# Optimization experiments

Hardware: AMD Instinct MI355X
Metric: run time of the kernel (lower is better)

Reference implementation:

```python
import jax, jax.numpy as jnp
import numpy as np

N_NODES = 100000
N_EDGES = 1600000
IN_FEATS = 256
H_FEATS = 128
N_CLASSES = 40


def setup_inputs() -> dict:
    key = jax.random.key(0)
    ks = jax.random.split(key, 6)
    in_feat = jax.random.normal(ks[0], (N_NODES, IN_FEATS), dtype=jnp.float32)
    src = jax.random.randint(ks[1], (N_EDGES,), 0, N_NODES, dtype=jnp.int32)
    dst = jax.random.randint(ks[2], (N_EDGES,), 0, N_NODES, dtype=jnp.int32)
    # Glorot-ish init for the two GraphConv weights
    W1 = jax.random.normal(ks[3], (IN_FEATS, H_FEATS), dtype=jnp.float32) * (1.0 / np.sqrt(IN_FEATS))
    b1 = jnp.zeros((H_FEATS,), dtype=jnp.float32)
    W2 = jax.random.normal(ks[4], (H_FEATS, N_CLASSES), dtype=jnp.float32) * (1.0 / np.sqrt(H_FEATS))
    b2 = jnp.zeros((N_CLASSES,), dtype=jnp.float32)
    return {"in_feat": in_feat, "src": src, "dst": dst,
            "W1": W1, "b1": b1, "W2": W2, "b2": b2}


def _degree_isqrt(idx, n):
    # degree per node, clamped to >=1 (DGL norm='both' behavior), then ^-1/2
    deg = jax.ops.segment_sum(jnp.ones_like(idx, dtype=jnp.float32), idx, num_segments=n)
    return jax.lax.rsqrt(jnp.maximum(deg, 1.0))


def _graph_conv(x, W, b, src, dst, out_isqrt, in_isqrt, n):
    # DGL GraphConv norm='both', weight applied before aggregation
    h = (x @ W) * out_isqrt[:, None]            # [N, F_out]
    m = jax.ops.segment_sum(h[src], dst, num_segments=n)  # gather+scatter over edges
    return m * in_isqrt[:, None] + b


def reference(in_feat, src, dst, W1, b1, W2, b2):
    n = in_feat.shape[0]
    out_isqrt = _degree_isqrt(src, n)  # out-degree norm for source nodes
    in_isqrt = _degree_isqrt(dst, n)   # in-degree norm for destination nodes
    h = _graph_conv(in_feat, W1, b1, src, dst, out_isqrt, in_isqrt, n)
    h = jax.nn.relu(h)
    h = _graph_conv(h, W2, b2, src, dst, out_isqrt, in_isqrt, n)
    return h
```

## Files before the change

### kernel.cpp

```cpp
#include <hip/hip_runtime.h>
#include <hip/hip_bf16.h>
#include <stdint.h>

#define NN 100000
#define NE 1600000
#define INF 256
#define HF 128
#define NC 40
#define NNP 100352
#define NBUK 1568
#define BKSH 6
#define NBLK 256
#define CHUNK 6250
#define SA 1536
#define SB 1536

typedef unsigned short ushort_t;
typedef unsigned int uint_t;
typedef unsigned char uchar_t;
typedef __attribute__((ext_vector_type(8))) short short8;
typedef __attribute__((ext_vector_type(4))) float f32x4;

__device__ __forceinline__ float bflo(uint_t u) {
    union { uint_t i; float f; } v; v.i = u << 16; return v.f;
}
__device__ __forceinline__ float bfhi(uint_t u) {
    union { uint_t i; float f; } v; v.i = u & 0xffff0000u; return v.f;
}
__device__ __forceinline__ uint_t f2bf(float f) {
    __hip_bfloat16 h = __float2bfloat16(f);
    return (uint_t)*reinterpret_cast<ushort_t*>(&h);
}

__global__ void k_binit(uint_t* __restrict__ cursA, uint_t* __restrict__ cursB) {
    int t = blockIdx.x * 256 + threadIdx.x;
    if (t < NBUK) { cursA[t] = (uint_t)t * SA; cursB[t] = (uint_t)t * SB; }
}

__launch_bounds__(1024)
__global__ void k_bfill(const int* __restrict__ src, const int* __restrict__ dst,
                        uint_t* __restrict__ cursA, uint_t* __restrict__ cursB,
                        uint_t* __restrict__ edgesA, uchar_t* __restrict__ bytesB,
                        const float* __restrict__ W1, ushort_t* __restrict__ W1f,
                        const float* __restrict__ W2, ushort_t* __restrict__ W2f) {
    __shared__ uint_t hA[NBUK], hB[NBUK];
    for (int t = threadIdx.x; t < NBUK; t += 1024) { hA[t] = 0; hB[t] = 0; }

    int i = blockIdx.x * 1024 + threadIdx.x;
    if (i < INF * HF) {
        int k = i >> 7, n = i & 127;
        int ks = k >> 5, q = (k >> 3) & 3, j = k & 7;
        int ct = n >> 4, ln = n & 15;
        W1f[(((ks * 8 + ct) * 4 + q) * 16 + ln) * 8 + j] = (ushort_t)f2bf(W1[i]);
    }
    if (i < HF * 48) {
        int k = i / 48, n = i % 48;
        int ks = k >> 5, q = (k >> 3) & 3, j = k & 7;
        int ct = n >> 4, ln = n & 15;
        float v = (n < NC) ? W2[k * NC + n] : 0.0f;
        W2f[(((ks * 3 + ct) * 4 + q) * 16 + ln) * 8 + j] = (ushort_t)f2bf(v);
    }
    __syncthreads();

    const int beg = blockIdx.x * CHUNK, end = beg + CHUNK;
    for (int e = beg + threadIdx.x; e < end; e += 1024) {
        atomicAdd(&hA[(uint_t)dst[e] >> BKSH], 1u);
        atomicAdd(&hB[(uint_t)src[e] >> BKSH], 1u);
    }
    __syncthreads();
    for (int t = threadIdx.x; t < NBUK; t += 1024) {
        uint_t c = hA[t];
        hA[t] = c ? atomicAdd(&cursA[t], c) : 0;
        c = hB[t];
        hB[t] = c ? atomicAdd(&cursB[t], c) : 0;
    }
    __syncthreads();
    for (int e = beg + threadIdx.x; e < end; e += 1024) {
        uint_t d = (uint_t)dst[e], s = (uint_t)src[e];
        uint_t pA = atomicAdd(&hA[d >> BKSH], 1u);
        edgesA[pA] = ((d & 63u) << 17) | s;
        uint_t pB = atomicAdd(&hB[s >> BKSH], 1u);
        bytesB[pB] = (uchar_t)(s & 63u);
    }
}

__launch_bounds__(256)
__global__ void k_bfinish(const uint_t* __restrict__ cursA, const uint_t* __restrict__ cursB,
                          const uint_t* __restrict__ edgesA, const uchar_t* __restrict__ bytesB,
                          int* __restrict__ row_ptr, int* __restrict__ srcs,
                          float* __restrict__ isq_d, float* __restrict__ isq_s) {
    __shared__ uint_t red[256];
    __shared__ uint_t h[64], sc[64], cur[64];
    const int b = blockIdx.x, t = threadIdx.x;

    uint_t acc = 0;
    for (int i = t; i < b; i += 256) acc += cursA[i] - (uint_t)i * SA;
    red[t] = acc;
    __syncthreads();
    for (int off = 128; off > 0; off >>= 1) {
        if (t < off) red[t] += red[t + off];
        __syncthreads();
    }
    const uint_t obase = red[0];

    if (t < 64) h[t] = 0;
    __syncthreads();
    const uint_t begI = (uint_t)b * SA;
    const uint_t endI = cursA[b];
    for (uint_t e = begI + t; e < endI; e += 256)
        atomicAdd(&h[(edgesA[e] >> 17) & 63u], 1u);
    __syncthreads();
    uint_t v = (t < 64) ? h[t] : 0;
    if (t < 64) sc[t] = v;
    __syncthreads();
    for (int off = 1; off < 64; off <<= 1) {
        uint_t tv = (t >= off && t < 64) ? sc[t - off] : 0;
        __syncthreads();
        if (t < 64) sc[t] += tv;
        __syncthreads();
    }
    if (t < 64) {
        uint_t excl = sc[t] - v;
        row_ptr[b * 64 + t] = (int)(obase + excl);
        isq_d[b * 64 + t] = rsqrtf(fmaxf((float)v, 1.0f));
        cur[t] = excl;
    }
    __syncthreads();
    for (uint_t e = begI + t; e < endI; e += 256) {
        uint_t u = edgesA[e];
        uint_t p = atomicAdd(&cur[(u >> 17) & 63u], 1u);
        srcs[obase + p] = (int)(u & 0x1FFFFu);
    }
    __syncthreads();
    if (t < 64) h[t] = 0;
    __syncthreads();
    const uint_t begB = (uint_t)b * SB;
    const uint_t endB = cursB[b];
    for (uint_t e = begB + t; e < endB; e += 256)
        atomicAdd(&h[bytesB[e]], 1u);
    __syncthreads();
    if (t < 64) isq_s[b * 64 + t] = rsqrtf(fmaxf((float)h[t], 1.0f));
}

__launch_bounds__(256, 4)
__global__ void k_gemm1(const float* __restrict__ X, const ushort_t* __restrict__ W1f,
                        const float* __restrict__ isq_s, ushort_t* __restrict__ H) {
    const int wv = threadIdx.x >> 6;
    const int lane = threadIdx.x & 63;
    const int ln = lane & 15;
    const int q  = lane >> 4;
    const int r0 = blockIdx.x * 64 + wv * 16;
    const int rm = min(r0 + ln, NN - 1);

    f32x4 acc[8];
#pragma unroll
    for (int ct = 0; ct < 8; ++ct) acc[ct] = (f32x4){0.f, 0.f, 0.f, 0.f};

    const float* xp = &X[(size_t)rm * INF + q * 8];
    const uint4* wf = (const uint4*)W1f;

#pragma unroll
    for (int hf = 0; hf < 2; ++hf) {
        float4 xv[8];
#pragma unroll
        for (int t = 0; t < 4; ++t) {
            xv[2 * t]     = *(const float4*)(xp + (hf * 4 + t) * 32);
            xv[2 * t + 1] = *(const float4*)(xp + (hf * 4 + t) * 32 + 4);
        }
        short8 af[4];
#pragma unroll
        for (int t = 0; t < 4; ++t) {
            af[t][0] = (short)f2bf(xv[2 * t].x);
            af[t][1] = (short)f2bf(xv[2 * t].y);
            af[t][2] = (short)f2bf(xv[2 * t].z);
            af[t][3] = (short)f2bf(xv[2 * t].w);
            af[t][4] = (short)f2bf(xv[2 * t + 1].x);
            af[t][5] = (short)f2bf(xv[2 * t + 1].y);
            af[t][6] = (short)f2bf(xv[2 * t + 1].z);
            af[t][7] = (short)f2bf(xv[2 * t + 1].w);
        }
#pragma unroll
        for (int ks = 0; ks < 4; ++ks) {
#pragma unroll
            for (int ct = 0; ct < 8; ++ct) {
                union { uint4 u; short8 s; } bv;
                bv.u = wf[(size_t)((hf * 4 + ks) * 8 + ct) * 64 + lane];
                acc[ct] = __builtin_amdgcn_mfma_f32_16x16x32_bf16(af[ks], bv.s, acc[ct], 0, 0, 0);
            }
        }
    }

#pragma unroll
    for (int reg = 0; reg < 4; ++reg) {
        int r = r0 + q * 4 + reg;
        if (r < NN) {
            float s = isq_s[r];
#pragma unroll
            for (int ct = 0; ct < 8; ++ct)
                H[(size_t)r * HF + ct * 16 + ln] = (ushort_t)f2bf(acc[ct][reg] * s);
        }
    }
}

#define ACC8(v) { a[0] += bflo((v).x); a[1] += bfhi((v).x); \
                  a[2] += bflo((v).y); a[3] += bfhi((v).y); \
                  a[4] += bflo((v).z); a[5] += bfhi((v).z); \
                  a[6] += bflo((v).w); a[7] += bfhi((v).w); }

__launch_bounds__(256)
__global__ void k_agg1_gemm2(const int* __restrict__ row_ptr, const int* __restrict__ srcs,
                             const uint4* __restrict__ H16, const float* __restrict__ isq_d,
                             const float* __restrict__ isq_s, const float* __restrict__ b1,
                             const ushort_t* __restrict__ W2f, ushort_t* __restrict__ H2b) {
    __shared__ uint4 h1s[16][16];
    const int wv = threadIdx.x >> 6;
    const int lane = threadIdx.x & 63;
    const int grp = lane >> 4;
    const int gl  = lane & 15;
    const int n0 = blockIdx.x * 16;

    const float4 bva = ((const float4*)b1)[gl * 2];
    const float4 bvb = ((const float4*)b1)[gl * 2 + 1];

    for (int ni = 0; ni < 4; ++ni) {
        const int rl = wv * 4 + ni;
        const int n = n0 + rl;
        float a[8];
#pragma unroll
        for (int k = 0; k < 8; ++k) a[k] = 0.0f;

        int beg = row_ptr[n], end = row_ptr[n + 1];
        int j = beg;
        for (; j + 16 <= end; j += 16) {
            int sA = srcs[j + grp];
            int sB = srcs[j + 4 + grp];
            int sC = srcs[j + 8 + grp];
            int sD = srcs[j + 12 + grp];
            uint4 vA = H16[(size_t)sA * 16 + gl];
            uint4 vB = H16[(size_t)sB * 16 + gl];
            uint4 vC = H16[(size_t)sC * 16 + gl];
            uint4 vD = H16[(size_t)sD * 16 + gl];
            ACC8(vA); ACC8(vB); ACC8(vC); ACC8(vD);
        }
        for (; j + 8 <= end; j += 8) {
            int sA = srcs[j + grp];
            int sB = srcs[j + 4 + grp];
            uint4 vA = H16[(size_t)sA * 16 + gl];
            uint4 vB = H16[(size_t)sB * 16 + gl];
            ACC8(vA); ACC8(vB);
        }
        for (; j + 4 <= end; j += 4) {
            uint4 v = H16[(size_t)srcs[j + grp] * 16 + gl];
            ACC8(v);
        }
        int r = end - j;
        if (grp < r) {
            uint4 v = H16[(size_t)srcs[j + grp] * 16 + gl];
            ACC8(v);
        }
#pragma unroll
        for (int k = 0; k < 8; ++k) {
            a[k] += __shfl_xor(a[k], 16);
            a[k] += __shfl_xor(a[k], 32);
        }
        if (lane < 16) {
            float sc = isq_d[n];
            uint_t p0 = f2bf(fmaxf(a[0] * sc + bva.x, 0.0f))
                      | (f2bf(fmaxf(a[1] * sc + bva.y, 0.0f)) << 16);
            uint_t p1 = f2bf(fmaxf(a[2] * sc + bva.z, 0.0f))
                      | (f2bf(fmaxf(a[3] * sc + bva.w, 0.0f)) << 16);
            uint_t p2 = f2bf(fmaxf(a[4] * sc + bvb.x, 0.0f))
                      | (f2bf(fmaxf(a[5] * sc + bvb.y, 0.0f)) << 16);
            uint_t p3 = f2bf(fmaxf(a[6] * sc + bvb.z, 0.0f))
                      | (f2bf(fmaxf(a[7] * sc + bvb.w, 0.0f)) << 16);
            h1s[rl][gl ^ rl] = (uint4){p0, p1, p2, p3};
        }
    }
    __syncthreads();

    if (wv < 3) {
        const int q = grp;
        const int ln = gl;
        f32x4 acc = (f32x4){0.f, 0.f, 0.f, 0.f};
        const uint4* wf = (const uint4*)W2f;
#pragma unroll
        for (int ks = 0; ks < 4; ++ks) {
            union { uint4 u; short8 s; } av, bv;
            av.u = h1s[ln][(ks * 4 + q) ^ ln];
            bv.u = wf[(size_t)(ks * 3 + wv) * 64 + lane];
            acc = __builtin_amdgcn_mfma_f32_16x16x32_bf16(av.s, bv.s, acc, 0, 0, 0);
        }
        int c = wv * 16 + ln;
        if (c < NC) {
#pragma unroll
            for (int reg = 0; reg < 4; ++reg) {
                int rg = n0 + q * 4 + reg;
                H2b[(size_t)rg * NC + c] = (ushort_t)f2bf(acc[reg] * isq_s[rg]);
            }
        }
    }
}

__launch_bounds__(256)
__global__ void k_gather2(const int* __restrict__ row_ptr, const int* __restrict__ srcs,
                          const uint4* __restrict__ H2b4, const float* __restrict__ isq_d,
                          const float* __restrict__ b2, float* __restrict__ out) {
    __shared__ float pt[4][64][9];
    const int wv = threadIdx.x >> 6;
    const int lane = threadIdx.x & 63;
    const int grp = lane / 5;
    const int gl  = lane - grp * 5;
    const int n = blockIdx.x * 4 + wv;

    float a[8];
#pragma unroll
    for (int k = 0; k < 8; ++k) a[k] = 0.0f;

    if (n < NN && grp < 12) {
        int beg = row_ptr[n], end = row_ptr[n + 1];
        int j = beg;
        for (; j + 24 <= end; j += 24) {
            int sA = srcs[j + grp];
            int sB = srcs[j + 12 + grp];
            uint4 vA = H2b4[(size_t)sA * 5 + gl];
            uint4 vB = H2b4[(size_t)sB * 5 + gl];
            ACC8(vA); ACC8(vB);
        }
        if (j + 12 <= end) {
            uint4 v = H2b4[(size_t)srcs[j + grp] * 5 + gl];
            ACC8(v);
            j += 12;
        }
        int r = end - j;
        if (grp < r) {
            uint4 v = H2b4[(size_t)srcs[j + grp] * 5 + gl];
            ACC8(v);
        }
    }
#pragma unroll
    for (int k = 0; k < 8; ++k) pt[wv][lane][k] = a[k];
    __syncthreads();

    if (n < NN && lane < NC) {
        const int g2 = lane >> 3;
        const int i2 = lane & 7;
        float s = 0.0f;
#pragma unroll
        for (int g = 0; g < 12; ++g)
            s += pt[wv][g * 5 + g2][i2];
        out[(size_t)n * NC + lane] = s * isq_d[n] + b2[lane];
    }
}

extern "C" void kernel_launch(void* const* d_in, const int* in_sizes, int n_in,
                              void* d_out, int out_size, void* d_ws, size_t ws_size,
                              hipStream_t stream) {
    const float* X  = (const float*)d_in[0];
    const int* src  = (const int*)d_in[1];
    const int* dst  = (const int*)d_in[2];
    const float* W1 = (const float*)d_in[3];
    const float* b1 = (const float*)d_in[4];
    const float* W2 = (const float*)d_in[5];
    const float* b2 = (const float*)d_in[6];
    float* out = (float*)d_out;

    int* w = (int*)d_ws;
    uint_t* cursA   = (uint_t*)w;
    uint_t* cursB   = cursA + NBUK;
    float* isq_s    = (float*)(w + 4096);
    float* isq_d    = isq_s + NNP;
    int* row_ptr    = (int*)(isq_d + NNP);
    ushort_t* W1f   = (ushort_t*)(row_ptr + NNP);
    ushort_t* W2f   = (ushort_t*)(row_ptr + NNP + 16384);
    int* Hw         = row_ptr + NNP + 19456;
    uint_t* edgesA  = (uint_t*)Hw;
    uchar_t* bytesB = (uchar_t*)(Hw + NBUK * SA);
    ushort_t* H     = (ushort_t*)Hw;
    int* srcs       = Hw + 6400000;
    ushort_t* H2b   = (ushort_t*)(srcs + NE);

    k_binit <<<(NBUK + 255) / 256, 256, 0, stream>>>(cursA, cursB);
    k_bfill <<<NBLK, 1024, 0, stream>>>(src, dst, cursA, cursB, edgesA, bytesB,
                                        W1, W1f, W2, W2f);
    k_bfinish<<<NBUK, 256, 0, stream>>>(cursA, cursB, edgesA, bytesB,
                                        row_ptr, srcs, isq_d, isq_s);

    k_gemm1<<<(NN + 63) / 64, 256, 0, stream>>>(X, W1f, isq_s, H);

    k_agg1_gemm2<<<NN / 16, 256, 0, stream>>>(row_ptr, srcs, (const uint4*)H,
                                              isq_d, isq_s, b1, W2f, H2b);

    k_gather2<<<(NN + 3) / 4, 256, 0, stream>>>(row_ptr, srcs, (const uint4*)H2b,
                                                isq_d, b2, out);
}
```

Measured before the change: 339.5 us.

## Slice H1 features into 16-column planes and split agg1 from gemm2

The layer-1 GEMM output is stored feature-sliced: eight planes of 16 columns, each NN rows by 32 bytes, instead of row-major 256-byte rows. The aggregation kernel gives each block a single slice, so gathered rows hit a smaller 3.2 MB working set that should stay in cache. The aggregated slice is written back in the same layout. The fused aggregation+GEMM2 kernel is split into a separate k_gemm2 pass, which adds an extra kernel launch and an extra round trip of h1 through memory. In exchange, each gather uses only 32-byte segments, and each edge's srcs index is reread eight times.

```diff
diff --git a/kernel.cpp b/kernel.cpp
--- a/kernel.cpp
+++ b/kernel.cpp
@@ -197,7 +197,7 @@
             float s = isq_s[r];
 #pragma unroll
             for (int ct = 0; ct < 8; ++ct)
-                H[(size_t)r * HF + ct * 16 + ln] = (ushort_t)f2bf(acc[ct][reg] * s);
+                H[((size_t)ct * NN + r) * 16 + ln] = (ushort_t)f2bf(acc[ct][reg] * s);
         }
     }
 }
@@ -208,94 +208,105 @@
                   a[6] += bflo((v).w); a[7] += bfhi((v).w); }
 
 __launch_bounds__(256)
-__global__ void k_agg1_gemm2(const int* __restrict__ row_ptr, const int* __restrict__ srcs,
-                             const uint4* __restrict__ H16, const float* __restrict__ isq_d,
-                             const float* __restrict__ isq_s, const float* __restrict__ b1,
-                             const ushort_t* __restrict__ W2f, ushort_t* __restrict__ H2b) {
-    __shared__ uint4 h1s[16][16];
+__global__ void k_agg1s(const int* __restrict__ row_ptr, const int* __restrict__ srcs,
+                        const uint4* __restrict__ Hfs, const float* __restrict__ isq_d,
+                        const float* __restrict__ b1, uint4* __restrict__ h1fs) {
     const int wv = threadIdx.x >> 6;
     const int lane = threadIdx.x & 63;
-    const int grp = lane >> 4;
-    const int gl  = lane & 15;
-    const int n0 = blockIdx.x * 16;
-
-    const float4 bva = ((const float4*)b1)[gl * 2];
-    const float4 bvb = ((const float4*)b1)[gl * 2 + 1];
-
-    for (int ni = 0; ni < 4; ++ni) {
-        const int rl = wv * 4 + ni;
-        const int n = n0 + rl;
+    const int hl = (lane >> 5) & 1;
+    const int slot = (lane >> 1) & 15;
+    const int half = lane & 1;
+    const int sl = blockIdx.x & 7;
+    const int chunk = blockIdx.x >> 3;
+    const size_t base = (size_t)sl * NN;
+
+    for (int pass = 0; pass < 10; ++pass) {
+        const int n = chunk * 80 + pass * 8 + wv * 2 + hl;
         float a[8];
 #pragma unroll
         for (int k = 0; k < 8; ++k) a[k] = 0.0f;
 
         int beg = row_ptr[n], end = row_ptr[n + 1];
         int j = beg;
-        for (; j + 16 <= end; j += 16) {
-            int sA = srcs[j + grp];
-            int sB = srcs[j + 4 + grp];
-            int sC = srcs[j + 8 + grp];
-            int sD = srcs[j + 12 + grp];
-            uint4 vA = H16[(size_t)sA * 16 + gl];
-            uint4 vB = H16[(size_t)sB * 16 + gl];
-            uint4 vC = H16[(size_t)sC * 16 + gl];
-            uint4 vD = H16[(size_t)sD * 16 + gl];
-            ACC8(vA); ACC8(vB); ACC8(vC); ACC8(vD);
-        }
-        for (; j + 8 <= end; j += 8) {
-            int sA = srcs[j + grp];
-            int sB = srcs[j + 4 + grp];
-            uint4 vA = H16[(size_t)sA * 16 + gl];
-            uint4 vB = H16[(size_t)sB * 16 + gl];
+        for (; j + 32 <= end; j += 32) {
+            int sA = srcs[j + slot];
+            int sB = srcs[j + 16 + slot];
+            uint4 vA = Hfs[(base + sA) * 2 + half];
+            uint4 vB = Hfs[(base + sB) * 2 + half];
             ACC8(vA); ACC8(vB);
         }
-        for (; j + 4 <= end; j += 4) {
-            uint4 v = H16[(size_t)srcs[j + grp] * 16 + gl];
+        if (j + 16 <= end) {
+            uint4 v = Hfs[(base + srcs[j + slot]) * 2 + half];
             ACC8(v);
-        }
-        int r = end - j;
-        if (grp < r) {
-            uint4 v = H16[(size_t)srcs[j + grp] * 16 + gl];
+            j += 16;
+        }
+        int rem = end - j;
+        if (slot < rem) {
+            uint4 v = Hfs[(base + srcs[j + slot]) * 2 + half];
             ACC8(v);
         }
 #pragma unroll
         for (int k = 0; k < 8; ++k) {
+            a[k] += __shfl_xor(a[k], 2);
+            a[k] += __shfl_xor(a[k], 4);
+            a[k] += __shfl_xor(a[k], 8);
             a[k] += __shfl_xor(a[k], 16);
-            a[k] += __shfl_xor(a[k], 32);
-        }
-        if (lane < 16) {
+        }
+        if (slot == 0) {
             float sc = isq_d[n];
-            uint_t p0 = f2bf(fmaxf(a[0] * sc + bva.x, 0.0f))
-                      | (f2bf(fmaxf(a[1] * sc + bva.y, 0.0f)) << 16);
-            uint_t p1 = f2bf(fmaxf(a[2] * sc + bva.z, 0.0f))
-                      | (f2bf(fmaxf(a[3] * sc + bva.w, 0.0f)) << 16);
-            uint_t p2 = f2bf(fmaxf(a[4] * sc + bvb.x, 0.0f))
-                      | (f2bf(fmaxf(a[5] * sc + bvb.y, 0.0f)) << 16);
-            uint_t p3 = f2bf(fmaxf(a[6] * sc + bvb.z, 0.0f))
-                      | (f2bf(fmaxf(a[7] * sc + bvb.w, 0.0f)) << 16);
-            h1s[rl][gl ^ rl] = (uint4){p0, p1, p2, p3};
-        }
-    }
-    __syncthreads();
-
-    if (wv < 3) {
-        const int q = grp;
-        const int ln = gl;
-        f32x4 acc = (f32x4){0.f, 0.f, 0.f, 0.f};
-        const uint4* wf = (const uint4*)W2f;
-#pragma unroll
-        for (int ks = 0; ks < 4; ++ks) {
-            union { uint4 u; short8 s; } av, bv;
-            av.u = h1s[ln][(ks * 4 + q) ^ ln];
-            bv.u = wf[(size_t)(ks * 3 + wv) * 64 + lane];
-            acc = __builtin_amdgcn_mfma_f32_16x16x32_bf16(av.s, bv.s, acc, 0, 0, 0);
-        }
-        int c = wv * 16 + ln;
+            const int f0 = sl * 16 + half * 8;
+            float4 ba = *(const float4*)&b1[f0];
+            float4 bb = *(const float4*)&b1[f0 + 4];
+            uint_t p0 = f2bf(fmaxf(a[0] * sc + ba.x, 0.0f))
+                      | (f2bf(fmaxf(a[1] * sc + ba.y, 0.0f)) << 16);
+            uint_t p1 = f2bf(fmaxf(a[2] * sc + ba.z, 0.0f))
+                      | (f2bf(fmaxf(a[3] * sc + ba.w, 0.0f)) << 16);
+            uint_t p2 = f2bf(fmaxf(a[4] * sc + bb.x, 0.0f))
+                      | (f2bf(fmaxf(a[5] * sc + bb.y, 0.0f)) << 16);
+            uint_t p3 = f2bf(fmaxf(a[6] * sc + bb.z, 0.0f))
+                      | (f2bf(fmaxf(a[7] * sc + bb.w, 0.0f)) << 16);
+            h1fs[(base + n) * 2 + half] = (uint4){p0, p1, p2, p3};
+        }
+    }
+}
+
+__launch_bounds__(256)
+__global__ void k_gemm2(const uint4* __restrict__ h1fs, const ushort_t* __restrict__ W2f,
+                        const float* __restrict__ isq_s, ushort_t* __restrict__ H2b) {
+    const int wv = threadIdx.x >> 6;
+    const int lane = threadIdx.x & 63;
+    const int ln = lane & 15;
+    const int q  = lane >> 4;
+    const int r0 = blockIdx.x * 64 + wv * 16;
+    const int rm = min(r0 + ln, NN - 1);
+
+    f32x4 acc[3];
+#pragma unroll
+    for (int ct = 0; ct < 3; ++ct) acc[ct] = (f32x4){0.f, 0.f, 0.f, 0.f};
+
+    const uint4* wf = (const uint4*)W2f;
+#pragma unroll
+    for (int ks = 0; ks < 4; ++ks) {
+        union { uint4 u; short8 s; } av;
+        const int sl2 = ks * 2 + (q >> 1);
+        av.u = h1fs[((size_t)sl2 * NN + rm) * 2 + (q & 1)];
+#pragma unroll
+        for (int ct = 0; ct < 3; ++ct) {
+            union { uint4 u; short8 s; } bv;
+            bv.u = wf[(size_t)(ks * 3 + ct) * 64 + lane];
+            acc[ct] = __builtin_amdgcn_mfma_f32_16x16x32_bf16(av.s, bv.s, acc[ct], 0, 0, 0);
+        }
+    }
+
+#pragma unroll
+    for (int ct = 0; ct < 3; ++ct) {
+        const int c = ct * 16 + ln;
         if (c < NC) {
 #pragma unroll
             for (int reg = 0; reg < 4; ++reg) {
-                int rg = n0 + q * 4 + reg;
-                H2b[(size_t)rg * NC + c] = (ushort_t)f2bf(acc[reg] * isq_s[rg]);
+                int rg = r0 + q * 4 + reg;
+                if (rg < NN)
+                    H2b[(size_t)rg * NC + c] = (ushort_t)f2bf(acc[ct][reg] * isq_s[rg]);
             }
         }
     }
@@ -375,9 +386,10 @@
     int* Hw         = row_ptr + NNP + 19456;
     uint_t* edgesA  = (uint_t*)Hw;
     uchar_t* bytesB = (uchar_t*)(Hw + NBUK * SA);
-    ushort_t* H     = (ushort_t*)Hw;
+    ushort_t* Hfs   = (ushort_t*)Hw;
     int* srcs       = Hw + 6400000;
     ushort_t* H2b   = (ushort_t*)(srcs + NE);
+    uint4* h1fs     = (uint4*)(srcs + NE + 2000000);
 
     k_binit <<<(NBUK + 255) / 256, 256, 0, stream>>>(cursA, cursB);
     k_bfill <<<NBLK, 1024, 0, stream>>>(src, dst, cursA, cursB, edgesA, bytesB,
@@ -385,10 +397,12 @@
     k_bfinish<<<NBUK, 256, 0, stream>>>(cursA, cursB, edgesA, bytesB,
                                         row_ptr, srcs, isq_d, isq_s);
 
-    k_gemm1<<<(NN + 63) / 64, 256, 0, stream>>>(X, W1f, isq_s, H);
-
-    k_agg1_gemm2<<<NN / 16, 256, 0, stream>>>(row_ptr, srcs, (const uint4*)H,
-                                              isq_d, isq_s, b1, W2f, H2b);
+    k_gemm1<<<(NN + 63) / 64, 256, 0, stream>>>(X, W1f, isq_s, Hfs);
+
+    k_agg1s<<<(NN / 80) * 8, 256, 0, stream>>>(row_ptr, srcs, (const uint4*)Hfs,
+                                               isq_d, b1, h1fs);
+
+    k_gemm2<<<(NN + 63) / 64, 256, 0, stream>>>((const uint4*)h1fs, W2f, isq_s, H2b);
 
     k_gather2<<<(NN + 3) / 4, 256, 0, stream>>>(row_ptr, srcs, (const uint4*)H2b,
                                                 isq_d, b2, out);
```

Result: slower. 428.9 us (+26.3%).
